# Kernel optimization log

Hardware: AMD Instinct MI355X
Metric: run time of the kernel (lower is better)

Reference implementation:

```python
import jax, jax.numpy as jnp
import numpy as np

EMBED_DIM = 512
NUM_HEADS = 8
HEAD_DIM = EMBED_DIM // NUM_HEADS
B, N, M = 4, 4096, 4096


def setup_inputs() -> dict:
    key = jax.random.key(0)
    ks = jax.random.split(key, 16)
    s = 0.02
    inp = {
        "query": jax.random.normal(ks[0], (B, N, EMBED_DIM), jnp.float32),
        "key": jax.random.normal(ks[1], (B, M, EMBED_DIM), jnp.float32),
        "value": jax.random.normal(ks[2], (B, M, EMBED_DIM), jnp.float32),
        # Linear weights stored as (in, out) so y = x @ W + b (== torch x @ W.T + b)
        "Wq": jax.random.normal(ks[3], (EMBED_DIM, EMBED_DIM), jnp.float32) * s,
        "bq": jnp.zeros((EMBED_DIM,), jnp.float32),
        "Wk": jax.random.normal(ks[4], (EMBED_DIM, EMBED_DIM), jnp.float32) * s,
        "bk": jnp.zeros((EMBED_DIM,), jnp.float32),
        "Wv": jax.random.normal(ks[5], (EMBED_DIM, EMBED_DIM), jnp.float32) * s,
        "bv": jnp.zeros((EMBED_DIM,), jnp.float32),
        # rank expansion MLP acts per-head on head_dim
        "W1": jax.random.normal(ks[6], (HEAD_DIM, HEAD_DIM * 2), jnp.float32) * s,
        "b1": jnp.zeros((HEAD_DIM * 2,), jnp.float32),
        "W2": jax.random.normal(ks[7], (HEAD_DIM * 2, HEAD_DIM), jnp.float32) * s,
        "b2": jnp.zeros((HEAD_DIM,), jnp.float32),
        "Wo": jax.random.normal(ks[8], (EMBED_DIM, EMBED_DIM), jnp.float32) * s,
        "bo": jnp.zeros((EMBED_DIM,), jnp.float32),
    }
    return inp


def reference(query, key, value, Wq, bq, Wk, bk, Wv, bv, W1, b1, W2, b2, Wo, bo):
    b, n, _ = query.shape
    m = key.shape[1]
    H, D = NUM_HEADS, HEAD_DIM
    # ELU+1 feature maps on projected q, k
    q = jax.nn.elu(query @ Wq + bq) + 1.0           # [B,N,E]
    k = jax.nn.elu(key @ Wk + bk) + 1.0             # [B,M,E]
    v = value @ Wv + bv                              # [B,M,E]
    q = q.reshape(b, n, H, D)
    k = k.reshape(b, m, H, D)
    v = v.reshape(b, m, H, D)
    # rank expansion MLP on keys (per head_dim), exact GELU as nn.GELU default
    k_aug = jax.nn.gelu(k @ W1 + b1, approximate=False) @ W2 + b2
    k_aug = jax.nn.elu(k_aug) + 1.0                  # [B,M,H,D]
    # inputs already fp32 (torch .float() casts are identity here)
    k_scaled = k_aug / m                             # normalize over context len
    kv_context = jnp.einsum('bmhd,bmhe->bhde', k_scaled, v)   # [B,H,D,D]
    out = jnp.einsum('bnhd,bhde->bnhe', q, kv_context)        # [B,N,H,D]
    k_sum = k_scaled.sum(axis=1)                      # [B,H,D]
    denom = jnp.einsum('bnhd,bhd->bnh', q, k_sum)     # [B,N,H]
    out = out / jnp.clip(denom, 1e-6, None)[..., None]
    out = jnp.clip(jnp.nan_to_num(out, nan=0.0, posinf=65000.0, neginf=-65000.0),
                   -65000.0, 65000.0)
    out = out.reshape(b, n, H * D)
    return out @ Wo + bo
```

## Files before the change

kernel.cpp:

```cpp
#include <hip/hip_runtime.h>
#include <hip/hip_bf16.h>
#include <cmath>

#define DEV __device__ __forceinline__

typedef __bf16 bf16x8 __attribute__((ext_vector_type(8)));
typedef float f32x4 __attribute__((ext_vector_type(4)));
typedef unsigned int u32;
typedef unsigned short u16;

DEV u16 f2bf(float f) {
  union { float f; u32 u; } v;
  v.f = f;
  u32 u = v.u;
  u += 0x7fffu + ((u >> 16) & 1u);
  return (u16)(u >> 16);
}
DEV u32 pk2(float a, float b) {
  union { __hip_bfloat162 h2; u32 u; } v;
  v.h2 = __float22bfloat162_rn(float2{a, b});
  return v.u;
}

DEV void async16(const void* g, void* l) {
  __builtin_amdgcn_global_load_lds((const __attribute__((address_space(1))) u32*)g,
                                   (__attribute__((address_space(3))) u32*)l, 16, 0, 0);
}

__global__ __launch_bounds__(256)
void qkv_gemm(const float* __restrict__ qin, const float* __restrict__ kin,
              const float* __restrict__ vin, const u16* __restrict__ WqT,
              const u16* __restrict__ WkT, const u16* __restrict__ WvT,
              const float* __restrict__ bq, const float* __restrict__ bk,
              const float* __restrict__ bv, u16* __restrict__ qact,
              u16* __restrict__ kact, u16* __restrict__ vT)
{
  __shared__ __align__(16) u16 SB[18432];
  float* Asf = (float*)SB;
  u16* Bs = SB + 8192;

  const int z = blockIdx.z;
  const float* Af = z == 0 ? qin : z == 1 ? kin : vin;
  const u16* Bt = z == 0 ? WqT : z == 1 ? WkT : WvT;
  const float* bias = z == 0 ? bq : z == 1 ? bk : bv;

  const int tid = threadIdx.x, wv = tid >> 6, lane = tid & 63;
  const int wr = wv >> 1, wc = wv & 1;
  const int lrow = lane & 15, lq = lane >> 4;
  const long r0 = (long)blockIdx.x * 128;
  const int c0 = blockIdx.y * 128;

  f32x4 acc[4][4] = {};

  for (int kt = 0; kt < 512; kt += 32) {
#pragma unroll
    for (int i = 0; i < 4; ++i) {
      const int s = (wv * 4 + i) * 64 + lane;
      const int row = s >> 3, p = s & 7;
      const int gp = p ^ (row & 7);
      async16(Af + (r0 + row) * 512 + kt + gp * 4, (char*)SB + (wv * 4 + i) * 1024);
    }
#pragma unroll
    for (int i = 0; i < 2; ++i) {
      const int s = (wv * 2 + i) * 64 + lane;
      async16(Bt + ((long)c0 + (s >> 2)) * 512 + kt + (s & 3) * 8,
              &Bs[(wv * 2 + i) * 512]);
    }
    __syncthreads();
    bf16x8 af[4], bfr[4];
#pragma unroll
    for (int i = 0; i < 4; ++i) {
      const int r = wr * 64 + i * 16 + lrow;
      const int r7 = r & 7, P0 = lq * 2;
      float4 lo = *(const float4*)&Asf[r * 32 + (P0 ^ r7) * 4];
      float4 hi = *(const float4*)&Asf[r * 32 + ((P0 + 1) ^ r7) * 4];
      union { u32 q[4]; bf16x8 v; } pk;
      pk.q[0] = pk2(lo.x, lo.y); pk.q[1] = pk2(lo.z, lo.w);
      pk.q[2] = pk2(hi.x, hi.y); pk.q[3] = pk2(hi.z, hi.w);
      af[i] = pk.v;
    }
#pragma unroll
    for (int j = 0; j < 4; ++j)
      bfr[j] = *(const bf16x8*)&Bs[(wc * 64 + j * 16 + lrow) * 32 + lq * 8];
#pragma unroll
    for (int i = 0; i < 4; ++i)
#pragma unroll
      for (int j = 0; j < 4; ++j)
        acc[i][j] = __builtin_amdgcn_mfma_f32_16x16x32_bf16(af[i], bfr[j], acc[i][j], 0, 0, 0);
    __syncthreads();
  }

  if (z < 2) {
    u16* Y = z == 0 ? qact : kact;
#pragma unroll
    for (int i = 0; i < 4; ++i) {
#pragma unroll
      for (int j = 0; j < 4; ++j) {
        const int col = c0 + wc * 64 + j * 16 + lrow;
        const float bvv = bias[col];
#pragma unroll
        for (int p = 0; p < 4; ++p) {
          float o = acc[i][j][p] + bvv;
          o = (o > 0.f) ? (o + 1.f) : __expf(o);
          const long row = r0 + wr * 64 + i * 16 + lq * 4 + p;
          Y[row * 512 + col] = f2bf(o);
        }
      }
    }
  } else {
    u16* LTv = SB + wv * 4608;
#pragma unroll
    for (int i = 0; i < 4; ++i) {
#pragma unroll
      for (int j = 0; j < 4; ++j) {
        const int col = c0 + wc * 64 + j * 16 + lrow;
        const float bvv = bias[col];
        ushort4 w;
        w.x = f2bf(acc[i][j][0] + bvv);
        w.y = f2bf(acc[i][j][1] + bvv);
        w.z = f2bf(acc[i][j][2] + bvv);
        w.w = f2bf(acc[i][j][3] + bvv);
        *(ushort4*)&LTv[(j * 16 + lrow) * 72 + i * 16 + lq * 4] = w;
      }
    }
    const int b = (int)(r0 >> 12);
    const int h = (c0 + wc * 64) >> 6;
    const int mg0 = (int)(r0 & 4095) + wr * 64;
#pragma unroll
    for (int ps = 0; ps < 8; ++ps) {
      const int e = ps * 8 + (lane >> 3);
      const int mq = (lane & 7) * 8;
      uint4 v = *(const uint4*)&LTv[e * 72 + mq];
      *(uint4*)(vT + (((long)b * 8 + h) * 64 + e) * 4096 + mg0 + mq) = v;
    }
  }
}

__global__ __launch_bounds__(256)
void out_gemm(const u16* __restrict__ A, const u16* __restrict__ Bt,
              const float* __restrict__ bias, float* __restrict__ Y)
{
  __shared__ __align__(16) u16 SB[8192];
  u16* As = SB;
  u16* Bs = SB + 4096;
  const int tid = threadIdx.x, wv = tid >> 6, lane = tid & 63;
  const int wr = wv >> 1, wc = wv & 1;
  const int lrow = lane & 15, lq = lane >> 4;
  const long r0 = (long)blockIdx.x * 128;
  const int c0 = blockIdx.y * 128;

  f32x4 acc[4][4] = {};
  for (int kt = 0; kt < 512; kt += 32) {
#pragma unroll
    for (int i = 0; i < 2; ++i) {
      const int s = (wv * 2 + i) * 64 + lane;
      async16(A + (r0 + (s >> 2)) * 512 + kt + (s & 3) * 8, &As[(wv * 2 + i) * 512]);
      async16(Bt + ((long)c0 + (s >> 2)) * 512 + kt + (s & 3) * 8, &Bs[(wv * 2 + i) * 512]);
    }
    __syncthreads();
    bf16x8 af[4], bfr[4];
#pragma unroll
    for (int i = 0; i < 4; ++i)
      af[i] = *(const bf16x8*)&As[(wr * 64 + i * 16 + lrow) * 32 + lq * 8];
#pragma unroll
    for (int j = 0; j < 4; ++j)
      bfr[j] = *(const bf16x8*)&Bs[(wc * 64 + j * 16 + lrow) * 32 + lq * 8];
#pragma unroll
    for (int i = 0; i < 4; ++i)
#pragma unroll
      for (int j = 0; j < 4; ++j)
        acc[i][j] = __builtin_amdgcn_mfma_f32_16x16x32_bf16(af[i], bfr[j], acc[i][j], 0, 0, 0);
    __syncthreads();
  }
#pragma unroll
  for (int i = 0; i < 4; ++i) {
#pragma unroll
    for (int j = 0; j < 4; ++j) {
      const int col = c0 + wc * 64 + j * 16 + lrow;
      const float bv = bias[col];
#pragma unroll
      for (int p = 0; p < 4; ++p) {
        const long row = r0 + wr * 64 + i * 16 + lq * 4 + p;
        Y[row * 512 + col] = acc[i][j][p] + bv;
      }
    }
  }
}

struct TArgs {
  const float* src[6];
  u16* dst[6];
  int K[6];
  int N[6];
};
__global__ __launch_bounds__(256)
void transpose_w(TArgs a)
{
  const int m = blockIdx.z;
  const int K = a.K[m], N = a.N[m];
  const int kt = blockIdx.y * 64, nt = blockIdx.x * 64;
  if (kt >= K || nt >= N) return;
  const float* src = a.src[m];
  u16* dst = a.dst[m];
  __shared__ u16 t[64][72];
  const int tx = threadIdx.x & 15, ty = threadIdx.x >> 4;
#pragma unroll
  for (int rr = 0; rr < 64; rr += 16) {
    const int k = kt + ty + rr;
    float4 v = *(const float4*)(src + (long)k * N + nt + tx * 4);
    t[tx * 4 + 0][ty + rr] = f2bf(v.x);
    t[tx * 4 + 1][ty + rr] = f2bf(v.y);
    t[tx * 4 + 2][ty + rr] = f2bf(v.z);
    t[tx * 4 + 3][ty + rr] = f2bf(v.w);
  }
  __syncthreads();
#pragma unroll
  for (int it = 0; it < 2; ++it) {
    const int s = threadIdx.x + it * 256;
    const int r = s >> 3, c = (s & 7) * 8;
    ushort4 u0 = *(ushort4*)&t[r][c];
    ushort4 u1 = *(ushort4*)&t[r][c + 4];
    *(ushort4*)(dst + (long)(nt + r) * K + kt + c) = u0;
    *(ushort4*)(dst + (long)(nt + r) * K + kt + c + 4) = u1;
  }
}

__global__ __launch_bounds__(256)
void mlp_fused(const u16* __restrict__ kact, const u16* __restrict__ W1T,
               const u16* __restrict__ W2T, const float* __restrict__ b1,
               const float* __restrict__ b2, u16* __restrict__ kaT, float invM)
{
  __shared__ __align__(16) u16 SB[27136];
  u16* As  = SB;
  u16* W1p = SB + 9216;
  u16* W2p = SB + 18432;
  u16* hid = SB;
  u16* LT2 = SB;

  const int tid = threadIdx.x, wv = tid >> 6, lane = tid & 63;
  const int lrow = lane & 15, lq = lane >> 4;
  const int bh = blockIdx.y, b = bh >> 3, h = bh & 7;
  const int m0 = blockIdx.x * 128;
  const long kbase = ((long)b * 4096 + m0) * 512 + h * 64;

#pragma unroll
  for (int i = 0; i < 4; ++i) {
    const int c = i * 256 + tid;
    const int row = c >> 3, p = c & 7;
    uint4 v = *(const uint4*)(kact + kbase + (long)row * 512 + p * 8);
    *(uint4*)&As[row * 72 + p * 8] = v;
  }
#pragma unroll
  for (int i = 0; i < 4; ++i) {
    const int c = i * 256 + tid;
    const int row = c >> 3, p = c & 7;
    uint4 v = *(const uint4*)(W1T + c * 8);
    *(uint4*)&W1p[row * 72 + p * 8] = v;
  }
#pragma unroll
  for (int i = 0; i < 4; ++i) {
    const int c = i * 256 + tid;
    const int row = c >> 4, p = c & 15;
    uint4 v = *(const uint4*)(W2T + c * 8);
    *(uint4*)&W2p[row * 136 + p * 8] = v;
  }
  __syncthreads();

  const int c0 = (wv >> 1) * 64, mh0 = (wv & 1) * 64;
  f32x4 acc1[4][4] = {};
#pragma unroll
  for (int kt = 0; kt < 2; ++kt) {
    bf16x8 wa[4], kb[4];
#pragma unroll
    for (int i = 0; i < 4; ++i)
      wa[i] = *(const bf16x8*)&W1p[(c0 + i * 16 + lrow) * 72 + kt * 32 + lq * 8];
#pragma unroll
    for (int j = 0; j < 4; ++j)
      kb[j] = *(const bf16x8*)&As[(mh0 + j * 16 + lrow) * 72 + kt * 32 + lq * 8];
#pragma unroll
    for (int i = 0; i < 4; ++i)
#pragma unroll
      for (int j = 0; j < 4; ++j)
        acc1[i][j] = __builtin_amdgcn_mfma_f32_16x16x32_bf16(wa[i], kb[j], acc1[i][j], 0, 0, 0);
  }
  __syncthreads();

#pragma unroll
  for (int i = 0; i < 4; ++i) {
    const int cc = c0 + i * 16 + lq * 4;
    float4 bv = *(const float4*)(b1 + cc);
#pragma unroll
    for (int j = 0; j < 4; ++j) {
      const int m = mh0 + j * 16 + lrow;
      float x0 = acc1[i][j][0] + bv.x, x1 = acc1[i][j][1] + bv.y;
      float x2 = acc1[i][j][2] + bv.z, x3 = acc1[i][j][3] + bv.w;
      ushort4 w;
      w.x = f2bf(0.5f * x0 * (1.f + erff(x0 * 0.7071067811865475f)));
      w.y = f2bf(0.5f * x1 * (1.f + erff(x1 * 0.7071067811865475f)));
      w.z = f2bf(0.5f * x2 * (1.f + erff(x2 * 0.7071067811865475f)));
      w.w = f2bf(0.5f * x3 * (1.f + erff(x3 * 0.7071067811865475f)));
      *(ushort4*)&hid[m * 136 + cc] = w;
    }
  }
  __syncthreads();

  const int d0 = (wv >> 1) * 32, mh2 = (wv & 1) * 64;
  f32x4 acc2[4][2] = {};
#pragma unroll
  for (int kt = 0; kt < 4; ++kt) {
    bf16x8 wa[2], hb[4];
#pragma unroll
    for (int i = 0; i < 2; ++i)
      wa[i] = *(const bf16x8*)&W2p[(d0 + i * 16 + lrow) * 136 + kt * 32 + lq * 8];
#pragma unroll
    for (int j = 0; j < 4; ++j)
      hb[j] = *(const bf16x8*)&hid[(mh2 + j * 16 + lrow) * 136 + kt * 32 + lq * 8];
#pragma unroll
    for (int j = 0; j < 4; ++j)
#pragma unroll
      for (int i = 0; i < 2; ++i)
        acc2[j][i] = __builtin_amdgcn_mfma_f32_16x16x32_bf16(hb[j], wa[i], acc2[j][i], 0, 0, 0);
  }
  __syncthreads();

#pragma unroll
  for (int i = 0; i < 2; ++i) {
    const int d = d0 + i * 16 + lrow;
    const float bd = b2[d];
#pragma unroll
    for (int j = 0; j < 4; ++j) {
      const int ml = mh2 + j * 16 + lq * 4;
      ushort4 w;
#pragma unroll
      for (int p = 0; p < 4; ++p) {
        float v = acc2[j][i][p] + bd;
        v = ((v > 0.f) ? (v + 1.f) : __expf(v)) * invM;
        ((u16*)&w)[p] = f2bf(v);
      }
      *(ushort4*)&LT2[d * 136 + ml] = w;
    }
  }
  __syncthreads();
#pragma unroll
  for (int it = 0; it < 4; ++it) {
    const int c = it * 256 + tid;
    const int d = c >> 4, mq = (c & 15) * 8;
    uint4 v = *(const uint4*)&LT2[d * 136 + mq];
    *(uint4*)(kaT + ((long)bh * 64 + d) * 4096 + m0 + mq) = v;
  }
}

__global__ __launch_bounds__(256)
void kv_gemm(const u16* __restrict__ kaT, const u16* __restrict__ vT,
             float* __restrict__ kvp, float* __restrict__ ksp)
{
  const int sp = blockIdx.x;
  const int bh = blockIdx.y;
  __shared__ u16 SB[16384];
  u16* As = SB;
  u16* Bs = SB + 8192;
  const int tid = threadIdx.x, wv = tid >> 6, lane = tid & 63;
  const int lrow = lane & 15, lq = lane >> 4;
  f32x4 acc[4][4] = {};
  f32x4 accs[4] = {};
  bf16x8 ones;
#pragma unroll
  for (int z = 0; z < 8; ++z) ones[z] = (__bf16)1.0f;
  const long base = (long)bh * 64 * 4096;

  for (int ph = 0; ph < 2; ++ph) {
    const int m0 = sp * 256 + ph * 128;
#pragma unroll
    for (int i = 0; i < 4; ++i) {
      const int s = (wv * 4 + i) * 64 + lane;
      const int chunk = s >> 8, row = (s >> 2) & 63, part = s & 3;
      const long g = base + (long)row * 4096 + m0 + chunk * 32 + part * 8;
      async16(kaT + g, &As[(wv * 4 + i) * 512]);
      async16(vT + g, &Bs[(wv * 4 + i) * 512]);
    }
    __syncthreads();
    bf16x8 af[4], bfr[4];
#pragma unroll
    for (int i = 0; i < 4; ++i)
      af[i] = *(const bf16x8*)&As[wv * 2048 + (i * 16 + lrow) * 32 + lq * 8];
#pragma unroll
    for (int j = 0; j < 4; ++j)
      bfr[j] = *(const bf16x8*)&Bs[wv * 2048 + (j * 16 + lrow) * 32 + lq * 8];
#pragma unroll
    for (int i = 0; i < 4; ++i) {
#pragma unroll
      for (int j = 0; j < 4; ++j)
        acc[i][j] = __builtin_amdgcn_mfma_f32_16x16x32_bf16(af[i], bfr[j], acc[i][j], 0, 0, 0);
      accs[i] = __builtin_amdgcn_mfma_f32_16x16x32_bf16(af[i], ones, accs[i], 0, 0, 0);
    }
    __syncthreads();
  }

  float* red = (float*)SB;
  float* ksr = red + 64 * 68;
  for (int w = 0; w < 4; ++w) {
    __syncthreads();
    if (wv == w) {
#pragma unroll
      for (int i = 0; i < 4; ++i) {
#pragma unroll
        for (int j = 0; j < 4; ++j) {
          const int e = j * 16 + lrow, dd = i * 16 + lq * 4;
          float* p = &red[e * 68 + dd];
          if (w == 0) { p[0] = acc[i][j][0]; p[1] = acc[i][j][1]; p[2] = acc[i][j][2]; p[3] = acc[i][j][3]; }
          else        { p[0] += acc[i][j][0]; p[1] += acc[i][j][1]; p[2] += acc[i][j][2]; p[3] += acc[i][j][3]; }
        }
        if (lrow == 0) {
          const int dd = i * 16 + lq * 4;
#pragma unroll
          for (int p2 = 0; p2 < 4; ++p2) {
            if (w == 0) ksr[dd + p2] = accs[i][p2];
            else        ksr[dd + p2] += accs[i][p2];
          }
        }
      }
    }
  }
  __syncthreads();
  float* kvo = kvp + ((long)sp * 32 + bh) * 4096;
  for (int s = tid; s < 4096; s += 256) kvo[s] = red[(s >> 6) * 68 + (s & 63)];
  if (tid < 64) ksp[(sp * 32 + bh) * 64 + tid] = ksr[tid];
}

__global__ __launch_bounds__(256)
void kv_reduce(const float* __restrict__ kvp, const float* __restrict__ ksp,
               u16* __restrict__ kvT, u16* __restrict__ ksumT)
{
  const int bh = blockIdx.x;
  const int t = threadIdx.x;
  for (int s = t; s < 4096; s += 256) {
    float v = 0.f;
#pragma unroll
    for (int sp = 0; sp < 16; ++sp) v += kvp[((long)sp * 32 + bh) * 4096 + s];
    kvT[(long)bh * 4096 + s] = f2bf(v);
  }
  if (t < 64) {
    float v = 0.f;
#pragma unroll
    for (int sp = 0; sp < 16; ++sp) v += ksp[(sp * 32 + bh) * 64 + t];
    ksumT[bh * 64 + t] = f2bf(v);
  }
}

__global__ __launch_bounds__(256)
void attn_mfma(const u16* __restrict__ q, const u16* __restrict__ kvT,
               const u16* __restrict__ ksumT, u16* __restrict__ attn)
{
  __shared__ u16 SB[17408];
  const int tid = threadIdx.x, wv = tid >> 6, lane = tid & 63;
  const int lrow = lane & 15, lq = lane >> 4;
  const int n0 = blockIdx.x * 256;
  const int bh = blockIdx.y, b = bh >> 3, h = bh & 7;
  u16* As = SB;

#pragma unroll
  for (int half = 0; half < 2; ++half)
#pragma unroll
    for (int i = 0; i < 4; ++i) {
      const int s = (wv * 4 + i) * 64 + lane;
      async16(q + ((long)(b * 4096 + n0 + (s >> 2))) * 512 + h * 64 + half * 32 + (s & 3) * 8,
              &As[half * 8192 + (wv * 4 + i) * 512]);
    }
  bf16x8 bfr[2][4], ks[2];
#pragma unroll
  for (int half = 0; half < 2; ++half) {
#pragma unroll
    for (int j = 0; j < 4; ++j)
      bfr[half][j] = *(const bf16x8*)(kvT + ((long)bh * 64 + j * 16 + lrow) * 64 + half * 32 + lq * 8);
    ks[half] = *(const bf16x8*)(ksumT + bh * 64 + half * 32 + lq * 8);
  }
  __syncthreads();

  f32x4 acc[4][4] = {};
  f32x4 accd[4] = {};
#pragma unroll
  for (int half = 0; half < 2; ++half) {
    bf16x8 af[4];
#pragma unroll
    for (int i = 0; i < 4; ++i)
      af[i] = *(const bf16x8*)&As[half * 8192 + (wv * 64 + i * 16 + lrow) * 32 + lq * 8];
#pragma unroll
    for (int i = 0; i < 4; ++i) {
#pragma unroll
      for (int j = 0; j < 4; ++j)
        acc[i][j] = __builtin_amdgcn_mfma_f32_16x16x32_bf16(af[i], bfr[half][j], acc[i][j], 0, 0, 0);
      accd[i] = __builtin_amdgcn_mfma_f32_16x16x32_bf16(af[i], ks[half], accd[i], 0, 0, 0);
    }
  }
  __syncthreads();

  u16* LT = SB;
#pragma unroll
  for (int i = 0; i < 4; ++i) {
    float dinv[4];
#pragma unroll
    for (int p = 0; p < 4; ++p) dinv[p] = 1.f / fmaxf(accd[i][p], 1e-6f);
#pragma unroll
    for (int j = 0; j < 4; ++j) {
      const int e = j * 16 + lrow;
      const int nl0 = i * 16 + lq * 4;
      ushort4 w;
      float x0 = acc[i][j][0] * dinv[0], x1 = acc[i][j][1] * dinv[1];
      float x2 = acc[i][j][2] * dinv[2], x3 = acc[i][j][3] * dinv[3];
      if (!(x0 == x0)) x0 = 0.f;
      if (!(x1 == x1)) x1 = 0.f;
      if (!(x2 == x2)) x2 = 0.f;
      if (!(x3 == x3)) x3 = 0.f;
      w.x = f2bf(fminf(65000.f, fmaxf(-65000.f, x0)));
      w.y = f2bf(fminf(65000.f, fmaxf(-65000.f, x1)));
      w.z = f2bf(fminf(65000.f, fmaxf(-65000.f, x2)));
      w.w = f2bf(fminf(65000.f, fmaxf(-65000.f, x3)));
      *(ushort4*)&LT[wv * 4352 + e * 68 + nl0] = w;
    }
  }
  __syncthreads();
#pragma unroll
  for (int it = 0; it < 8; ++it) {
    const int c = it * 256 + tid;
    const int n = c & 255, ec = c >> 8;
    const int wr2 = n >> 6, nl = n & 63;
    ushort4 w0, w1;
    w0.x = LT[wr2 * 4352 + (ec * 8 + 0) * 68 + nl];
    w0.y = LT[wr2 * 4352 + (ec * 8 + 1) * 68 + nl];
    w0.z = LT[wr2 * 4352 + (ec * 8 + 2) * 68 + nl];
    w0.w = LT[wr2 * 4352 + (ec * 8 + 3) * 68 + nl];
    w1.x = LT[wr2 * 4352 + (ec * 8 + 4) * 68 + nl];
    w1.y = LT[wr2 * 4352 + (ec * 8 + 5) * 68 + nl];
    w1.z = LT[wr2 * 4352 + (ec * 8 + 6) * 68 + nl];
    w1.w = LT[wr2 * 4352 + (ec * 8 + 7) * 68 + nl];
    u16* dst = attn + ((long)(b * 4096 + n0 + n)) * 512 + h * 64 + ec * 8;
    *(ushort4*)dst = w0;
    *(ushort4*)(dst + 4) = w1;
  }
}

static constexpr long U = 8388608;

extern "C" void kernel_launch(void* const* d_in, const int* in_sizes, int n_in,
                              void* d_out, int out_size, void* d_ws, size_t ws_size,
                              hipStream_t stream)
{
  const float* query = (const float*)d_in[0];
  const float* key   = (const float*)d_in[1];
  const float* value = (const float*)d_in[2];
  const float* Wq = (const float*)d_in[3];
  const float* bq = (const float*)d_in[4];
  const float* Wk = (const float*)d_in[5];
  const float* bk = (const float*)d_in[6];
  const float* Wv = (const float*)d_in[7];
  const float* bv = (const float*)d_in[8];
  const float* W1 = (const float*)d_in[9];
  const float* b1 = (const float*)d_in[10];
  const float* W2 = (const float*)d_in[11];
  const float* b2 = (const float*)d_in[12];
  const float* Wo = (const float*)d_in[13];
  const float* bo = (const float*)d_in[14];

  u16* wsh = (u16*)d_ws;
  u16* qact = wsh;
  u16* kact = wsh + U;
  u16* vT   = wsh + 2 * U;
  u16* kaT  = wsh + 3 * U;
  u16* attn = wsh + 4 * U;

  float* fp  = (float*)(wsh + 5 * U);
  float* kvp = fp;
  float* ksp = fp + 2097152;
  u16* kvTg   = (u16*)(fp + 2129920);
  u16* ksumTg = kvTg + 131072;
  u16* wtb = ksumTg + 2048;
  u16* WqT = wtb;
  u16* WkT = wtb + 262144;
  u16* WvT = wtb + 524288;
  u16* WoT = wtb + 786432;
  u16* W1T = wtb + 1048576;
  u16* W2T = wtb + 1056768;

  dim3 blk(256);
  const float invM = 1.f / 4096.f;

  TArgs ta;
  ta.src[0] = Wq; ta.dst[0] = WqT; ta.K[0] = 512; ta.N[0] = 512;
  ta.src[1] = Wk; ta.dst[1] = WkT; ta.K[1] = 512; ta.N[1] = 512;
  ta.src[2] = Wv; ta.dst[2] = WvT; ta.K[2] = 512; ta.N[2] = 512;
  ta.src[3] = Wo; ta.dst[3] = WoT; ta.K[3] = 512; ta.N[3] = 512;
  ta.src[4] = W1; ta.dst[4] = W1T; ta.K[4] = 64;  ta.N[4] = 128;
  ta.src[5] = W2; ta.dst[5] = W2T; ta.K[5] = 128; ta.N[5] = 64;
  transpose_w<<<dim3(8, 8, 6), blk, 0, stream>>>(ta);

  qkv_gemm<<<dim3(128, 4, 3), blk, 0, stream>>>(query, key, value, WqT, WkT, WvT,
                                                bq, bk, bv, qact, kact, vT);
  mlp_fused<<<dim3(32, 32), blk, 0, stream>>>(kact, W1T, W2T, b1, b2, kaT, invM);
  kv_gemm<<<dim3(16, 32), blk, 0, stream>>>(kaT, vT, kvp, ksp);
  kv_reduce<<<dim3(32), blk, 0, stream>>>(kvp, ksp, kvTg, ksumTg);
  attn_mfma<<<dim3(16, 32), blk, 0, stream>>>(qact, kvTg, ksumTg, attn);
  out_gemm<<<dim3(128, 4), blk, 0, stream>>>(attn, WoT, bo, (float*)d_out);
}
```

Before: 277.4 us.

## Pre-tile weights and attn output into swizzled blocks; widen GEMM K-tiles to 64

```diff
diff --git a/kernel.cpp b/kernel.cpp
--- a/kernel.cpp
+++ b/kernel.cpp
@@ -27,21 +27,23 @@
                                    (__attribute__((address_space(3))) u32*)l, 16, 0, 0);
 }
 
+DEV int swz(int row, int kq) { return row * 64 + ((kq * 8) ^ ((row & 7) << 3)); }
+
 __global__ __launch_bounds__(256)
 void qkv_gemm(const float* __restrict__ qin, const float* __restrict__ kin,
-              const float* __restrict__ vin, const u16* __restrict__ WqT,
-              const u16* __restrict__ WkT, const u16* __restrict__ WvT,
+              const float* __restrict__ vin, const u16* __restrict__ WqP,
+              const u16* __restrict__ WkP, const u16* __restrict__ WvP,
               const float* __restrict__ bq, const float* __restrict__ bk,
               const float* __restrict__ bv, u16* __restrict__ qact,
               u16* __restrict__ kact, u16* __restrict__ vT)
 {
   __shared__ __align__(16) u16 SB[18432];
-  float* Asf = (float*)SB;
+  u16* As = SB;
   u16* Bs = SB + 8192;
 
   const int z = blockIdx.z;
   const float* Af = z == 0 ? qin : z == 1 ? kin : vin;
-  const u16* Bt = z == 0 ? WqT : z == 1 ? WkT : WvT;
+  const u16* Bp = z == 0 ? WqP : z == 1 ? WkP : WvP;
   const float* bias = z == 0 ? bq : z == 1 ? bk : bv;
 
   const int tid = threadIdx.x, wv = tid >> 6, lane = tid & 63;
@@ -52,43 +54,53 @@
 
   f32x4 acc[4][4] = {};
 
-  for (int kt = 0; kt < 512; kt += 32) {
-#pragma unroll
-    for (int i = 0; i < 4; ++i) {
-      const int s = (wv * 4 + i) * 64 + lane;
-      const int row = s >> 3, p = s & 7;
-      const int gp = p ^ (row & 7);
-      async16(Af + (r0 + row) * 512 + kt + gp * 4, (char*)SB + (wv * 4 + i) * 1024);
-    }
-#pragma unroll
-    for (int i = 0; i < 2; ++i) {
-      const int s = (wv * 2 + i) * 64 + lane;
-      async16(Bt + ((long)c0 + (s >> 2)) * 512 + kt + (s & 3) * 8,
-              &Bs[(wv * 2 + i) * 512]);
+  for (int kt8 = 0; kt8 < 8; ++kt8) {
+    const int kt = kt8 * 64;
+    float4 fa[4][2];
+#pragma unroll
+    for (int it = 0; it < 4; ++it) {
+      const int s = it * 256 + tid;
+      const int row = s >> 3, kq = s & 7;
+      const float* g = Af + (r0 + row) * 512 + kt + kq * 8;
+      fa[it][0] = *(const float4*)g;
+      fa[it][1] = *(const float4*)(g + 4);
+    }
+    if (kt8) __syncthreads();
+#pragma unroll
+    for (int it = 0; it < 4; ++it) {
+      const int sl = it * 256 + wv * 64;
+      async16(Bp + ((long)blockIdx.y * 8 + kt8) * 8192 + (sl + lane) * 8,
+              &Bs[sl * 8]);
+    }
+#pragma unroll
+    for (int it = 0; it < 4; ++it) {
+      const int s = it * 256 + tid;
+      const int row = s >> 3, kq = s & 7;
+      union { u32 q[4]; uint4 v; } pk;
+      pk.q[0] = pk2(fa[it][0].x, fa[it][0].y);
+      pk.q[1] = pk2(fa[it][0].z, fa[it][0].w);
+      pk.q[2] = pk2(fa[it][1].x, fa[it][1].y);
+      pk.q[3] = pk2(fa[it][1].z, fa[it][1].w);
+      *(uint4*)&As[swz(row, kq)] = pk.v;
     }
     __syncthreads();
-    bf16x8 af[4], bfr[4];
-#pragma unroll
-    for (int i = 0; i < 4; ++i) {
-      const int r = wr * 64 + i * 16 + lrow;
-      const int r7 = r & 7, P0 = lq * 2;
-      float4 lo = *(const float4*)&Asf[r * 32 + (P0 ^ r7) * 4];
-      float4 hi = *(const float4*)&Asf[r * 32 + ((P0 + 1) ^ r7) * 4];
-      union { u32 q[4]; bf16x8 v; } pk;
-      pk.q[0] = pk2(lo.x, lo.y); pk.q[1] = pk2(lo.z, lo.w);
-      pk.q[2] = pk2(hi.x, hi.y); pk.q[3] = pk2(hi.z, hi.w);
-      af[i] = pk.v;
-    }
-#pragma unroll
-    for (int j = 0; j < 4; ++j)
-      bfr[j] = *(const bf16x8*)&Bs[(wc * 64 + j * 16 + lrow) * 32 + lq * 8];
-#pragma unroll
-    for (int i = 0; i < 4; ++i)
+#pragma unroll
+    for (int subk = 0; subk < 2; ++subk) {
+      bf16x8 af[4], bfr[4];
+#pragma unroll
+      for (int i = 0; i < 4; ++i)
+        af[i] = *(const bf16x8*)&As[swz(wr * 64 + i * 16 + lrow, subk * 4 + lq)];
 #pragma unroll
       for (int j = 0; j < 4; ++j)
-        acc[i][j] = __builtin_amdgcn_mfma_f32_16x16x32_bf16(af[i], bfr[j], acc[i][j], 0, 0, 0);
-    __syncthreads();
-  }
+        bfr[j] = *(const bf16x8*)&Bs[swz(wc * 64 + j * 16 + lrow, subk * 4 + lq)];
+#pragma unroll
+      for (int i = 0; i < 4; ++i)
+#pragma unroll
+        for (int j = 0; j < 4; ++j)
+          acc[i][j] = __builtin_amdgcn_mfma_f32_16x16x32_bf16(af[i], bfr[j], acc[i][j], 0, 0, 0);
+    }
+  }
+  __syncthreads();
 
   if (z < 2) {
     u16* Y = z == 0 ? qact : kact;
@@ -140,9 +152,9 @@
 void out_gemm(const u16* __restrict__ A, const u16* __restrict__ Bt,
               const float* __restrict__ bias, float* __restrict__ Y)
 {
-  __shared__ __align__(16) u16 SB[8192];
+  __shared__ __align__(16) u16 SB[16384];
   u16* As = SB;
-  u16* Bs = SB + 4096;
+  u16* Bs = SB + 8192;
   const int tid = threadIdx.x, wv = tid >> 6, lane = tid & 63;
   const int wr = wv >> 1, wc = wv & 1;
   const int lrow = lane & 15, lq = lane >> 4;
@@ -150,27 +162,30 @@
   const int c0 = blockIdx.y * 128;
 
   f32x4 acc[4][4] = {};
-  for (int kt = 0; kt < 512; kt += 32) {
-#pragma unroll
-    for (int i = 0; i < 2; ++i) {
-      const int s = (wv * 2 + i) * 64 + lane;
-      async16(A + (r0 + (s >> 2)) * 512 + kt + (s & 3) * 8, &As[(wv * 2 + i) * 512]);
-      async16(Bt + ((long)c0 + (s >> 2)) * 512 + kt + (s & 3) * 8, &Bs[(wv * 2 + i) * 512]);
+  for (int kt8 = 0; kt8 < 8; ++kt8) {
+    if (kt8) __syncthreads();
+#pragma unroll
+    for (int it = 0; it < 4; ++it) {
+      const int sl = it * 256 + wv * 64;
+      async16(A + ((long)blockIdx.x * 8 + kt8) * 8192 + (sl + lane) * 8, &As[sl * 8]);
+      async16(Bt + ((long)blockIdx.y * 8 + kt8) * 8192 + (sl + lane) * 8, &Bs[sl * 8]);
     }
     __syncthreads();
-    bf16x8 af[4], bfr[4];
-#pragma unroll
-    for (int i = 0; i < 4; ++i)
-      af[i] = *(const bf16x8*)&As[(wr * 64 + i * 16 + lrow) * 32 + lq * 8];
-#pragma unroll
-    for (int j = 0; j < 4; ++j)
-      bfr[j] = *(const bf16x8*)&Bs[(wc * 64 + j * 16 + lrow) * 32 + lq * 8];
-#pragma unroll
-    for (int i = 0; i < 4; ++i)
+#pragma unroll
+    for (int subk = 0; subk < 2; ++subk) {
+      bf16x8 af[4], bfr[4];
+#pragma unroll
+      for (int i = 0; i < 4; ++i)
+        af[i] = *(const bf16x8*)&As[swz(wr * 64 + i * 16 + lrow, subk * 4 + lq)];
 #pragma unroll
       for (int j = 0; j < 4; ++j)
-        acc[i][j] = __builtin_amdgcn_mfma_f32_16x16x32_bf16(af[i], bfr[j], acc[i][j], 0, 0, 0);
-    __syncthreads();
+        bfr[j] = *(const bf16x8*)&Bs[swz(wc * 64 + j * 16 + lrow, subk * 4 + lq)];
+#pragma unroll
+      for (int i = 0; i < 4; ++i)
+#pragma unroll
+        for (int j = 0; j < 4; ++j)
+          acc[i][j] = __builtin_amdgcn_mfma_f32_16x16x32_bf16(af[i], bfr[j], acc[i][j], 0, 0, 0);
+    }
   }
 #pragma unroll
   for (int i = 0; i < 4; ++i) {
@@ -214,14 +229,30 @@
     t[tx * 4 + 3][ty + rr] = f2bf(v.w);
   }
   __syncthreads();
-#pragma unroll
-  for (int it = 0; it < 2; ++it) {
-    const int s = threadIdx.x + it * 256;
-    const int r = s >> 3, c = (s & 7) * 8;
-    ushort4 u0 = *(ushort4*)&t[r][c];
-    ushort4 u1 = *(ushort4*)&t[r][c + 4];
-    *(ushort4*)(dst + (long)(nt + r) * K + kt + c) = u0;
-    *(ushort4*)(dst + (long)(nt + r) * K + kt + c + 4) = u1;
+  if (m < 4) {
+    const int ktile = kt >> 6;
+#pragma unroll
+    for (int it = 0; it < 2; ++it) {
+      const int s = threadIdx.x + it * 256;
+      const int r = s >> 3, c = (s & 7) * 8;
+      const int n = nt + r;
+      const int colblk = n >> 7, cl = n & 127;
+      ushort4 u0 = *(ushort4*)&t[r][c];
+      ushort4 u1 = *(ushort4*)&t[r][c + 4];
+      u16* d = dst + ((long)colblk * 8 + ktile) * 8192 + cl * 64 + (c ^ ((cl & 7) << 3));
+      *(ushort4*)d = u0;
+      *(ushort4*)(d + 4) = u1;
+    }
+  } else {
+#pragma unroll
+    for (int it = 0; it < 2; ++it) {
+      const int s = threadIdx.x + it * 256;
+      const int r = s >> 3, c = (s & 7) * 8;
+      ushort4 u0 = *(ushort4*)&t[r][c];
+      ushort4 u1 = *(ushort4*)&t[r][c + 4];
+      *(ushort4*)(dst + (long)(nt + r) * K + kt + c) = u0;
+      *(ushort4*)(dst + (long)(nt + r) * K + kt + c + 4) = u1;
+    }
   }
 }
 
@@ -433,13 +464,16 @@
 {
   const int bh = blockIdx.x;
   const int t = threadIdx.x;
-  for (int s = t; s < 4096; s += 256) {
+  const int s0 = blockIdx.y * 512;
+#pragma unroll
+  for (int i = 0; i < 2; ++i) {
+    const int s = s0 + i * 256 + t;
     float v = 0.f;
 #pragma unroll
     for (int sp = 0; sp < 16; ++sp) v += kvp[((long)sp * 32 + bh) * 4096 + s];
     kvT[(long)bh * 4096 + s] = f2bf(v);
   }
-  if (t < 64) {
+  if (blockIdx.y == 0 && t < 64) {
     float v = 0.f;
 #pragma unroll
     for (int sp = 0; sp < 16; ++sp) v += ksp[(sp * 32 + bh) * 64 + t];
@@ -533,7 +567,9 @@
     w1.y = LT[wr2 * 4352 + (ec * 8 + 5) * 68 + nl];
     w1.z = LT[wr2 * 4352 + (ec * 8 + 6) * 68 + nl];
     w1.w = LT[wr2 * 4352 + (ec * 8 + 7) * 68 + nl];
-    u16* dst = attn + ((long)(b * 4096 + n0 + n)) * 512 + h * 64 + ec * 8;
+    const int ng = b * 4096 + n0 + n;
+    const int rowblk = ng >> 7, rl = ng & 127;
+    u16* dst = attn + ((long)rowblk * 8 + h) * 8192 + rl * 64 + ((ec * 8) ^ ((rl & 7) << 3));
     *(ushort4*)dst = w0;
     *(ushort4*)(dst + 4) = w1;
   }
@@ -597,7 +633,7 @@
                                                 bq, bk, bv, qact, kact, vT);
   mlp_fused<<<dim3(32, 32), blk, 0, stream>>>(kact, W1T, W2T, b1, b2, kaT, invM);
   kv_gemm<<<dim3(16, 32), blk, 0, stream>>>(kaT, vT, kvp, ksp);
-  kv_reduce<<<dim3(32), blk, 0, stream>>>(kvp, ksp, kvTg, ksumTg);
+  kv_reduce<<<dim3(32, 8), blk, 0, stream>>>(kvp, ksp, kvTg, ksumTg);
   attn_mfma<<<dim3(16, 32), blk, 0, stream>>>(qact, kvTg, ksumTg, attn);
   out_gemm<<<dim3(128, 4), blk, 0, stream>>>(attn, WoT, bo, (float*)d_out);
 }
```

Result: faster. 254.4 us (-8.3%).
